# Optimization experiments

Measured on AMD Instinct MI355X. Metric: run time of the kernel, lower is better.

Reference implementation:

```python
import jax, jax.numpy as jnp
import numpy as np

B = 1_000_000   # reflections
K = 16_384      # groups
E = 64          # encoder_out
H = 64          # hidden_dim


def setup_inputs() -> dict:
    key = jax.random.key(0)
    ks = jax.random.split(key, 12)
    x = jax.random.normal(ks[0], (B, E), dtype=jnp.float32)
    gl = jax.random.randint(ks[1], (B,), 0, K)
    # guarantee every group id 0..K-1 appears, so torch.unique == arange(K)
    gl = gl.at[:K].set(jnp.arange(K))
    s = 0.05
    W1 = jax.random.normal(ks[2], (E, H), jnp.float32) * s
    b1 = jax.random.normal(ks[3], (H,), jnp.float32) * s
    W2 = jax.random.normal(ks[4], (H, H), jnp.float32) * s
    b2 = jax.random.normal(ks[5], (H,), jnp.float32) * s
    W3 = jax.random.normal(ks[6], (H, H), jnp.float32) * s
    b3 = jax.random.normal(ks[7], (H,), jnp.float32) * s
    w_mu = jax.random.normal(ks[8], (H, 1), jnp.float32) * s
    b_mu = jnp.full((1,), -6.9, jnp.float32)   # log_tau_init
    w_lv = jax.random.normal(ks[9], (H, 1), jnp.float32) * s
    b_lv = jnp.full((1,), -2.0, jnp.float32)
    return {"x": x, "group_labels": gl, "W1": W1, "b1": b1, "W2": W2, "b2": b2,
            "W3": W3, "b3": b3, "w_mu": w_mu, "b_mu": b_mu, "w_lv": w_lv, "b_lv": b_lv}


def reference(x, group_labels, W1, b1, W2, b2, W3, b3, w_mu, b_mu, w_lv, b_lv):
    # phi: Linear -> SiLU -> Linear -> SiLU
    z = jax.nn.silu(jax.nn.silu(x @ W1 + b1) @ W2 + b2)          # (B, H)
    # segment mean by group (math-equivalent to the dense one-hot matmul)
    counts = jax.ops.segment_sum(jnp.ones((z.shape[0],), z.dtype),
                                 group_labels, num_segments=K)    # (K,)
    gsum = jax.ops.segment_sum(z, group_labels, num_segments=K)   # (K, H)
    group_features = gsum / counts[:, None]
    # rho + heads
    h = jax.nn.silu(group_features @ W3 + b3)                     # (K, H)
    mu = (h @ w_mu + b_mu)[:, 0]                                  # (K,)
    logvar = jnp.clip((h @ w_lv + b_lv)[:, 0], -10.0, 4.0)        # (K,)
    std = jnp.exp(0.5 * logvar)
    eps = jax.random.normal(jax.random.key(42), std.shape, std.dtype)
    log_tau = mu + std * eps                                      # reparam sample
    tau_group = jnp.exp(log_tau)
    # unique_groups == arange(K) by construction -> searchsorted is identity
    tau_per_refl = tau_group[group_labels][:, None]               # (B, 1)
    log_tau_per_refl = log_tau[group_labels][:, None]             # (B, 1)
    return (mu, logvar, tau_per_refl, log_tau_per_refl)
```

## Files before the change

kernel.cpp:

```cpp
#include <hip/hip_runtime.h>

#define BN 1000000
#define KN 16384
#define HN 64
#define TPB 256
#define NW  4
#define NB  512
#define NCHUNK ((BN + TPB - 1) / TPB)

typedef __bf16 bf16x8 __attribute__((ext_vector_type(8)));
typedef float  f32x4  __attribute__((ext_vector_type(4)));
typedef unsigned short u16x8 __attribute__((ext_vector_type(8)));

__device__ __forceinline__ unsigned short f2bf(float f) {
    unsigned u = __float_as_uint(f);
    u += 0x7fffu + ((u >> 16) & 1u);
    return (unsigned short)(u >> 16);
}
__device__ __forceinline__ float bf2f(unsigned short b) {
    return __uint_as_float(((unsigned)b) << 16);
}
__device__ __forceinline__ float silu_f(float v) {
    return v * __builtin_amdgcn_rcpf(1.0f + __expf(-v));
}
__device__ __forceinline__ f32x4 mfma16(bf16x8 a, bf16x8 b, f32x4 c) {
    return __builtin_amdgcn_mfma_f32_16x16x32_bf16(a, b, c, 0, 0, 0);
}

__device__ __forceinline__ float erfinv_xla(float x) {
    float w = -log1pf(-x * x);
    float p;
    if (w < 5.0f) {
        w -= 2.5f;
        p = 2.81022636e-08f;
        p = fmaf(p, w, 3.43273939e-07f);
        p = fmaf(p, w, -3.5233877e-06f);
        p = fmaf(p, w, -4.39150654e-06f);
        p = fmaf(p, w, 0.00021858087f);
        p = fmaf(p, w, -0.00125372503f);
        p = fmaf(p, w, -0.00417768164f);
        p = fmaf(p, w, 0.246640727f);
        p = fmaf(p, w, 1.50140941f);
    } else {
        w = sqrtf(w) - 3.0f;
        p = -0.000200214257f;
        p = fmaf(p, w, 0.000100950558f);
        p = fmaf(p, w, 0.00134934322f);
        p = fmaf(p, w, -0.00367342844f);
        p = fmaf(p, w, 0.00573950773f);
        p = fmaf(p, w, -0.0076224613f);
        p = fmaf(p, w, 0.00943887047f);
        p = fmaf(p, w, 1.00167406f);
        p = fmaf(p, w, 2.83297682f);
    }
    return p * x;
}

__device__ __forceinline__ float jax_eps16384(int gid) {
    const unsigned k0 = 0u, k1 = 42u, k2 = 0x1BD11BDAu ^ 0u ^ 42u;
    unsigned x0 = 0u + k0;
    unsigned x1 = (unsigned)gid + k1;
#define TF_RND(r) { x0 += x1; x1 = (x1 << (r)) | (x1 >> (32 - (r))); x1 ^= x0; }
    TF_RND(13) TF_RND(15) TF_RND(26) TF_RND(6)  x0 += k1; x1 += k2 + 1u;
    TF_RND(17) TF_RND(29) TF_RND(16) TF_RND(24) x0 += k2; x1 += k0 + 2u;
    TF_RND(13) TF_RND(15) TF_RND(26) TF_RND(6)  x0 += k0; x1 += k1 + 3u;
    TF_RND(17) TF_RND(29) TF_RND(16) TF_RND(24) x0 += k1; x1 += k2 + 4u;
    TF_RND(13) TF_RND(15) TF_RND(26) TF_RND(6)  x0 += k2; x1 += k0 + 5u;
#undef TF_RND
    unsigned bits = x0 ^ x1;
    float f = __uint_as_float((bits >> 9) | 0x3f800000u) - 1.0f;
    const float mn = -0.99999994f;
    float u = fmaxf(f * 2.0f + mn, mn);
    return 1.41421354f * erfinv_xla(u);
}

__global__ __launch_bounds__(256) void k_count(const int* __restrict__ gl,
                                               int* __restrict__ counts,
                                               float4* __restrict__ gz) {
    int i = blockIdx.x * 256 + threadIdx.x;
    const float4 z4 = make_float4(0.f, 0.f, 0.f, 0.f);
    for (int j = i; j < KN * HN / 4; j += 250112) gz[j] = z4;
    if (i < BN / 4) {
        int4 g = ((const int4*)gl)[i];
        atomicAdd(&counts[g.x], 1); atomicAdd(&counts[g.y], 1);
        atomicAdd(&counts[g.z], 1); atomicAdd(&counts[g.w], 1);
    }
}

__global__ __launch_bounds__(1024) void k_scan(const int* __restrict__ counts, int* __restrict__ cursor) {
    __shared__ int wtot[16];
    const int t = threadIdx.x, lane = t & 63, wv = t >> 6;
    const int4* c4 = (const int4*)counts;
    int4 q0 = c4[t * 4], q1 = c4[t * 4 + 1], q2 = c4[t * 4 + 2], q3 = c4[t * 4 + 3];
    int c[16] = {q0.x, q0.y, q0.z, q0.w, q1.x, q1.y, q1.z, q1.w,
                 q2.x, q2.y, q2.z, q2.w, q3.x, q3.y, q3.z, q3.w};
    int loc[16], s = 0;
    #pragma unroll
    for (int i = 0; i < 16; ++i) { loc[i] = s; s += c[i]; }
    const int own = s;
    #pragma unroll
    for (int off = 1; off < 64; off <<= 1) {
        int v = __shfl_up(s, off);
        if (lane >= off) s += v;
    }
    if (lane == 63) wtot[wv] = s;
    __syncthreads();
    int wbase = 0;
    #pragma unroll
    for (int w = 0; w < 16; ++w) wbase += (w < wv) ? wtot[w] : 0;
    const int ebase = wbase + s - own;
    int o[16];
    #pragma unroll
    for (int i = 0; i < 16; ++i) o[i] = ebase + loc[i];
    int4* o4 = (int4*)cursor;
    o4[t * 4]     = make_int4(o[0],  o[1],  o[2],  o[3]);
    o4[t * 4 + 1] = make_int4(o[4],  o[5],  o[6],  o[7]);
    o4[t * 4 + 2] = make_int4(o[8],  o[9],  o[10], o[11]);
    o4[t * 4 + 3] = make_int4(o[12], o[13], o[14], o[15]);
}

__global__ __launch_bounds__(256) void k_scatter(const int* __restrict__ gl, int* __restrict__ cursor,
                                                 int2* __restrict__ spk) {
    int i = blockIdx.x * 256 + threadIdx.x;
    if (i < BN / 4) {
        int4 g = ((const int4*)gl)[i];
        int r = i * 4;
        int p0 = atomicAdd(&cursor[g.x], 1); spk[p0] = make_int2(r,     g.x);
        int p1 = atomicAdd(&cursor[g.y], 1); spk[p1] = make_int2(r + 1, g.y);
        int p2 = atomicAdd(&cursor[g.z], 1); spk[p2] = make_int2(r + 2, g.z);
        int p3 = atomicAdd(&cursor[g.w], 1); spk[p3] = make_int2(r + 3, g.w);
    }
}

__global__ __launch_bounds__(TPB, 2) void k_phase1(
    const float* __restrict__ x, const int2* __restrict__ spk,
    const float* __restrict__ W1, const float* __restrict__ b1,
    const float* __restrict__ W2, const float* __restrict__ b2,
    float* __restrict__ gsum)
{
    __shared__ __align__(16) unsigned short w1t[64 * 64];
    __shared__ __align__(16) unsigned short w2t[64 * 64];
    __shared__ __align__(16) unsigned short xh[NW][64 * 64];
    __shared__ float b1s[64], b2s[64];
    __shared__ int sg_s[NW][64];

    const int t = threadIdx.x;
    const int wv = t >> 6, lane = t & 63;
    const int lj = lane & 15, lg = lane >> 4;

    {
        const float4* W1v = (const float4*)W1;
        const float4* W2v = (const float4*)W2;
        #pragma unroll
        for (int i = 0; i < 4; ++i) {
            int e4 = i * 256 + t;
            int k  = e4 >> 4;
            int j0 = (e4 & 15) * 4;
            float4 a = W1v[e4];
            float4 b = W2v[e4];
            float av[4] = {a.x, a.y, a.z, a.w};
            float bv[4] = {b.x, b.y, b.z, b.w};
            #pragma unroll
            for (int c = 0; c < 4; ++c) {
                int j = j0 + c;
                int off = j * 128 + ((2 * k) ^ ((j & 7) << 4));
                *(unsigned short*)((char*)w1t + off) = f2bf(av[c]);
                *(unsigned short*)((char*)w2t + off) = f2bf(bv[c]);
            }
        }
        if (t < 64) { b1s[t] = b1[t]; b2s[t] = b2[t]; }
    }
    __syncthreads();

    float bc1[4], bc2[4];
    #pragma unroll
    for (int ct = 0; ct < 4; ++ct) { bc1[ct] = b1s[ct * 16 + lj]; bc2[ct] = b2s[ct * 16 + lj]; }

    unsigned short* myx = &xh[wv][0];
    int2   rsA[4], rsB[4];
    float4 xr[4][4];
    bf16x8 af[4][2];

    auto load_spk = [&](int c, int2 (&dst)[4]) {
        int cc = c < NCHUNK - 1 ? c : NCHUNK - 1;
        #pragma unroll
        for (int rt = 0; rt < 4; ++rt) {
            int r = cc * TPB + wv * 64 + rt * 16 + lj;
            dst[rt] = spk[r < BN ? r : BN - 1];
        }
    };
    auto load_x = [&](const int2 (&src)[4]) {
        #pragma unroll
        for (int rt = 0; rt < 4; ++rt) {
            const float* xp = x + (size_t)src[rt].x * 64 + lg * 8;
            xr[rt][0] = *(const float4*)(xp);
            xr[rt][1] = *(const float4*)(xp + 4);
            xr[rt][2] = *(const float4*)(xp + 32);
            xr[rt][3] = *(const float4*)(xp + 36);
        }
    };
    auto compute = [&]() {
        f32x4 acc[4][4];
        #pragma unroll
        for (int a = 0; a < 4; ++a)
            #pragma unroll
            for (int b = 0; b < 4; ++b) acc[a][b] = f32x4{0.f, 0.f, 0.f, 0.f};
        #pragma unroll
        for (int kk = 0; kk < 2; ++kk) {
            const int kbyte = kk * 64 + lg * 16;
            bf16x8 bw[4];
            #pragma unroll
            for (int ct = 0; ct < 4; ++ct) {
                int row = ct * 16 + lj;
                bw[ct] = *(const bf16x8*)((char*)w1t + row * 128 + (kbyte ^ ((row & 7) << 4)));
            }
            #pragma unroll
            for (int rt = 0; rt < 4; ++rt)
                #pragma unroll
                for (int ct = 0; ct < 4; ++ct)
                    acc[rt][ct] = mfma16(af[rt][kk], bw[ct], acc[rt][ct]);
        }
        #pragma unroll
        for (int rt = 0; rt < 4; ++rt) {
            #pragma unroll
            for (int ct = 0; ct < 4; ++ct) {
                f32x4 v = acc[rt][ct];
                #pragma unroll
                for (int rg = 0; rg < 4; ++rg) {
                    int row = rt * 16 + lg * 4 + rg;
                    int col = ct * 16 + lj;
                    float h = silu_f(v[rg] + bc1[ct]);
                    int off = row * 128 + ((2 * col) ^ ((row & 7) << 4));
                    *(unsigned short*)((char*)myx + off) = f2bf(h);
                }
                acc[rt][ct] = f32x4{0.f, 0.f, 0.f, 0.f};
            }
        }
        #pragma unroll
        for (int kk = 0; kk < 2; ++kk) {
            const int kbyte = kk * 64 + lg * 16;
            bf16x8 bw[4];
            #pragma unroll
            for (int ct = 0; ct < 4; ++ct) {
                int row = ct * 16 + lj;
                bw[ct] = *(const bf16x8*)((char*)w2t + row * 128 + (kbyte ^ ((row & 7) << 4)));
            }
            #pragma unroll
            for (int rt = 0; rt < 4; ++rt) {
                int row = rt * 16 + lj;
                bf16x8 aw = *(const bf16x8*)((char*)myx + row * 128 + (kbyte ^ ((row & 7) << 4)));
                #pragma unroll
                for (int ct = 0; ct < 4; ++ct)
                    acc[rt][ct] = mfma16(aw, bw[ct], acc[rt][ct]);
            }
        }
        #pragma unroll
        for (int rt = 0; rt < 4; ++rt) {
            #pragma unroll
            for (int ct = 0; ct < 4; ++ct) {
                f32x4 v = acc[rt][ct];
                int col  = ct * 16 + lj;
                int row0 = rt * 16 + lg * 4;
                ushort4 pk;
                pk.x = f2bf(silu_f(v[0] + bc2[ct]));
                pk.y = f2bf(silu_f(v[1] + bc2[ct]));
                pk.z = f2bf(silu_f(v[2] + bc2[ct]));
                pk.w = f2bf(silu_f(v[3] + bc2[ct]));
                *(ushort4*)((char*)myx + col * 128 + ((2 * row0) ^ ((col & 7) << 4))) = pk;
            }
        }
        {
            const int c = lane;
            const char* zT = (const char*)myx;
            float vsum = 0.0f;
            int curg = -2;
            #pragma unroll
            for (int blk = 0; blk < 8; ++blk) {
                u16x8 v = *(const u16x8*)(zT + c * 128 + ((16 * blk) ^ ((c & 7) << 4)));
                int4 ga = *(const int4*)(&sg_s[wv][blk * 8]);
                int4 gb = *(const int4*)(&sg_s[wv][blk * 8 + 4]);
                int gs[8] = {ga.x, ga.y, ga.z, ga.w, gb.x, gb.y, gb.z, gb.w};
                #pragma unroll
                for (int j = 0; j < 8; ++j) {
                    int g = gs[j];
                    if (g != curg) {
                        if (curg >= 0) atomicAdd(&gsum[curg * 64 + c], vsum);
                        vsum = 0.0f;
                        curg = g;
                    }
                    vsum += bf2f(v[j]);
                }
            }
            if (curg >= 0) atomicAdd(&gsum[curg * 64 + c], vsum);
        }
    };

    auto pstep = [&](int2 (&CUR)[4], int2 (&NXT)[4], int c) {
        if (lg == 0) {
            #pragma unroll
            for (int rt = 0; rt < 4; ++rt) {
                int r = c * TPB + wv * 64 + rt * 16 + lj;
                sg_s[wv][rt * 16 + lj] = (r < BN) ? CUR[rt].y : -1;
            }
        }
        #pragma unroll
        for (int rt = 0; rt < 4; ++rt)
            #pragma unroll
            for (int kk = 0; kk < 2; ++kk) {
                float4 a = xr[rt][kk * 2], b = xr[rt][kk * 2 + 1];
                u16x8 u;
                u[0] = f2bf(a.x); u[1] = f2bf(a.y); u[2] = f2bf(a.z); u[3] = f2bf(a.w);
                u[4] = f2bf(b.x); u[5] = f2bf(b.y); u[6] = f2bf(b.z); u[7] = f2bf(b.w);
                af[rt][kk] = __builtin_bit_cast(bf16x8, u);
            }
        load_x(NXT);
        load_spk(c + 2 * NB, CUR);
        compute();
    };

    const int c0 = blockIdx.x;
    load_spk(c0, rsA);
    load_spk(c0 + NB, rsB);
    load_x(rsA);

    int c = c0;
    while (true) {
        pstep(rsA, rsB, c); c += NB; if (c >= NCHUNK) break;
        pstep(rsB, rsA, c); c += NB; if (c >= NCHUNK) break;
    }
}

__global__ __launch_bounds__(64) void k_phase2(
    const float* __restrict__ gsum, const int* __restrict__ counts,
    const float* __restrict__ W3, const float* __restrict__ b3,
    const float* __restrict__ wmu, const float* __restrict__ bmu,
    const float* __restrict__ wlv, const float* __restrict__ blv,
    float* __restrict__ out, float* __restrict__ taug, float* __restrict__ ltaug)
{
    __shared__ __align__(16) float w3t[64 * 64];
    __shared__ float b3s[64], wmus[64], wlvs[64];
    const int t = threadIdx.x;
    for (int i = 0; i < 64; ++i) w3t[t * 64 + i] = W3[i * 64 + t];
    b3s[t] = b3[t]; wmus[t] = wmu[t]; wlvs[t] = wlv[t];
    __syncthreads();

    const int gid = blockIdx.x * 64 + t;
    const float inv = 1.0f / (float)counts[gid];
    float gf[64];
    #pragma unroll
    for (int i = 0; i < 16; ++i) {
        float4 v = *(const float4*)(gsum + (size_t)gid * 64 + i * 4);
        gf[i * 4 + 0] = v.x * inv; gf[i * 4 + 1] = v.y * inv;
        gf[i * 4 + 2] = v.z * inv; gf[i * 4 + 3] = v.w * inv;
    }
    float mu = bmu[0], lv = blv[0];
    for (int j = 0; j < 64; ++j) {
        float a = b3s[j];
        const float4* wr = (const float4*)(w3t + j * 64);
        #pragma unroll
        for (int k = 0; k < 16; ++k) {
            float4 wv = wr[k];
            a += gf[k * 4 + 0] * wv.x + gf[k * 4 + 1] * wv.y
               + gf[k * 4 + 2] * wv.z + gf[k * 4 + 3] * wv.w;
        }
        float h = silu_f(a);
        mu += h * wmus[j];
        lv += h * wlvs[j];
    }
    lv = fminf(fmaxf(lv, -10.0f), 4.0f);
    float sd  = __expf(0.5f * lv);
    float eps = jax_eps16384(gid);
    float lt  = mu + sd * eps;
    out[gid]      = mu;
    out[KN + gid] = lv;
    taug[gid]  = __expf(lt);
    ltaug[gid] = lt;
}

__global__ __launch_bounds__(256) void k_phase3(
    const int* __restrict__ gl, const float* __restrict__ taug,
    const float* __restrict__ ltaug, float* __restrict__ out)
{
    int i = blockIdx.x * 256 + threadIdx.x;
    if (i < BN / 4) {
        int4 g = ((const int4*)gl)[i];
        float4 tv = make_float4(taug[g.x],  taug[g.y],  taug[g.z],  taug[g.w]);
        float4 lv = make_float4(ltaug[g.x], ltaug[g.y], ltaug[g.z], ltaug[g.w]);
        ((float4*)(out + 2 * KN))[i]      = tv;
        ((float4*)(out + 2 * KN + BN))[i] = lv;
    }
}

extern "C" void kernel_launch(void* const* d_in, const int* in_sizes, int n_in,
                              void* d_out, int out_size, void* d_ws, size_t ws_size,
                              hipStream_t stream)
{
    const float* x   = (const float*)d_in[0];
    const int*   gl  = (const int*)d_in[1];
    const float* W1  = (const float*)d_in[2];
    const float* b1  = (const float*)d_in[3];
    const float* W2  = (const float*)d_in[4];
    const float* b2  = (const float*)d_in[5];
    const float* W3  = (const float*)d_in[6];
    const float* b3  = (const float*)d_in[7];
    const float* wmu = (const float*)d_in[8];
    const float* bmu = (const float*)d_in[9];
    const float* wlv = (const float*)d_in[10];
    const float* blv = (const float*)d_in[11];
    float* out = (float*)d_out;

    float* ws     = (float*)d_ws;
    float* gsum   = ws;
    int*   counts = (int*)(gsum + KN * HN);
    int*   cursor = counts + KN;
    float* taug   = (float*)(cursor + KN);
    float* ltaug  = taug + KN;
    int2*  spk    = (int2*)(ltaug + KN);

    hipMemsetAsync(counts, 0, (size_t)KN * sizeof(int), stream);

    const int nb4 = (BN / 4 + 255) / 256;
    k_count  <<<nb4, 256, 0, stream>>>(gl, counts, (float4*)gsum);
    k_scan   <<<1, 1024, 0, stream>>>(counts, cursor);
    k_scatter<<<nb4, 256, 0, stream>>>(gl, cursor, spk);
    k_phase1 <<<NB, TPB, 0, stream>>>(x, spk, W1, b1, W2, b2, gsum);
    k_phase2 <<<KN / 64, 64, 0, stream>>>(gsum, counts, W3, b3, wmu, bmu, wlv, blv, out, taug, ltaug);
    k_phase3 <<<nb4, 256, 0, stream>>>(gl, taug, ltaug, out);
}
```

Measured before the change: 250.1 us.

## Drop x register prefetch and raise phase1 occupancy to three blocks per CU

Removes the software pipeline that held the next chunk's x rows in registers across the compute step. Now x is loaded at the start of each iteration, and only the sorted index pairs are prefetched one step ahead. Register pressure falls, which allows launch bounds of 3 blocks per SM/CU, and the grid grows from 512 to 768 blocks to match. The aim is to hide gather latency through more resident waves rather than in-thread prefetch. The risk is exposed load latency inside each wave if occupancy does not rise enough.

```diff
diff --git a/kernel.cpp b/kernel.cpp
--- a/kernel.cpp
+++ b/kernel.cpp
@@ -5,7 +5,7 @@
 #define HN 64
 #define TPB 256
 #define NW  4
-#define NB  512
+#define NB  768
 #define NCHUNK ((BN + TPB - 1) / TPB)
 
 typedef __bf16 bf16x8 __attribute__((ext_vector_type(8)));
@@ -132,7 +132,7 @@
     }
 }
 
-__global__ __launch_bounds__(TPB, 2) void k_phase1(
+__global__ __launch_bounds__(TPB, 3) void k_phase1(
     const float* __restrict__ x, const int2* __restrict__ spk,
     const float* __restrict__ W1, const float* __restrict__ b1,
     const float* __restrict__ W2, const float* __restrict__ b2,
@@ -177,9 +177,7 @@
     for (int ct = 0; ct < 4; ++ct) { bc1[ct] = b1s[ct * 16 + lj]; bc2[ct] = b2s[ct * 16 + lj]; }
 
     unsigned short* myx = &xh[wv][0];
-    int2   rsA[4], rsB[4];
-    float4 xr[4][4];
-    bf16x8 af[4][2];
+    int2 rsA[4], rsB[4];
 
     auto load_spk = [&](int c, int2 (&dst)[4]) {
         int cc = c < NCHUNK - 1 ? c : NCHUNK - 1;
@@ -189,17 +187,37 @@
             dst[rt] = spk[r < BN ? r : BN - 1];
         }
     };
-    auto load_x = [&](const int2 (&src)[4]) {
+
+    auto iter = [&](int2 (&CUR)[4], int2 (&NXT)[4], int c) {
+        float4 xr[4][4];
         #pragma unroll
         for (int rt = 0; rt < 4; ++rt) {
-            const float* xp = x + (size_t)src[rt].x * 64 + lg * 8;
+            const float* xp = x + (size_t)CUR[rt].x * 64 + lg * 8;
             xr[rt][0] = *(const float4*)(xp);
             xr[rt][1] = *(const float4*)(xp + 4);
             xr[rt][2] = *(const float4*)(xp + 32);
             xr[rt][3] = *(const float4*)(xp + 36);
         }
-    };
-    auto compute = [&]() {
+        load_spk(c + NB, NXT);
+        if (lg == 0) {
+            #pragma unroll
+            for (int rt = 0; rt < 4; ++rt) {
+                int r = c * TPB + wv * 64 + rt * 16 + lj;
+                sg_s[wv][rt * 16 + lj] = (r < BN) ? CUR[rt].y : -1;
+            }
+        }
+        bf16x8 af[4][2];
+        #pragma unroll
+        for (int rt = 0; rt < 4; ++rt)
+            #pragma unroll
+            for (int kk = 0; kk < 2; ++kk) {
+                float4 a = xr[rt][kk * 2], b = xr[rt][kk * 2 + 1];
+                u16x8 u;
+                u[0] = f2bf(a.x); u[1] = f2bf(a.y); u[2] = f2bf(a.z); u[3] = f2bf(a.w);
+                u[4] = f2bf(b.x); u[5] = f2bf(b.y); u[6] = f2bf(b.z); u[7] = f2bf(b.w);
+                af[rt][kk] = __builtin_bit_cast(bf16x8, u);
+            }
+
         f32x4 acc[4][4];
         #pragma unroll
         for (int a = 0; a < 4; ++a)
@@ -270,13 +288,13 @@
             }
         }
         {
-            const int c = lane;
+            const int c2 = lane;
             const char* zT = (const char*)myx;
             float vsum = 0.0f;
             int curg = -2;
             #pragma unroll
             for (int blk = 0; blk < 8; ++blk) {
-                u16x8 v = *(const u16x8*)(zT + c * 128 + ((16 * blk) ^ ((c & 7) << 4)));
+                u16x8 v = *(const u16x8*)(zT + c2 * 128 + ((16 * blk) ^ ((c2 & 7) << 4)));
                 int4 ga = *(const int4*)(&sg_s[wv][blk * 8]);
                 int4 gb = *(const int4*)(&sg_s[wv][blk * 8 + 4]);
                 int gs[8] = {ga.x, ga.y, ga.z, ga.w, gb.x, gb.y, gb.z, gb.w};
@@ -284,49 +302,22 @@
                 for (int j = 0; j < 8; ++j) {
                     int g = gs[j];
                     if (g != curg) {
-                        if (curg >= 0) atomicAdd(&gsum[curg * 64 + c], vsum);
+                        if (curg >= 0) atomicAdd(&gsum[curg * 64 + c2], vsum);
                         vsum = 0.0f;
                         curg = g;
                     }
                     vsum += bf2f(v[j]);
                 }
             }
-            if (curg >= 0) atomicAdd(&gsum[curg * 64 + c], vsum);
+            if (curg >= 0) atomicAdd(&gsum[curg * 64 + c2], vsum);
         }
     };
 
-    auto pstep = [&](int2 (&CUR)[4], int2 (&NXT)[4], int c) {
-        if (lg == 0) {
-            #pragma unroll
-            for (int rt = 0; rt < 4; ++rt) {
-                int r = c * TPB + wv * 64 + rt * 16 + lj;
-                sg_s[wv][rt * 16 + lj] = (r < BN) ? CUR[rt].y : -1;
-            }
-        }
-        #pragma unroll
-        for (int rt = 0; rt < 4; ++rt)
-            #pragma unroll
-            for (int kk = 0; kk < 2; ++kk) {
-                float4 a = xr[rt][kk * 2], b = xr[rt][kk * 2 + 1];
-                u16x8 u;
-                u[0] = f2bf(a.x); u[1] = f2bf(a.y); u[2] = f2bf(a.z); u[3] = f2bf(a.w);
-                u[4] = f2bf(b.x); u[5] = f2bf(b.y); u[6] = f2bf(b.z); u[7] = f2bf(b.w);
-                af[rt][kk] = __builtin_bit_cast(bf16x8, u);
-            }
-        load_x(NXT);
-        load_spk(c + 2 * NB, CUR);
-        compute();
-    };
-
-    const int c0 = blockIdx.x;
-    load_spk(c0, rsA);
-    load_spk(c0 + NB, rsB);
-    load_x(rsA);
-
-    int c = c0;
+    int c = blockIdx.x;
+    load_spk(c, rsA);
     while (true) {
-        pstep(rsA, rsB, c); c += NB; if (c >= NCHUNK) break;
-        pstep(rsB, rsA, c); c += NB; if (c >= NCHUNK) break;
+        iter(rsA, rsB, c); c += NB; if (c >= NCHUNK) break;
+        iter(rsB, rsA, c); c += NB; if (c >= NCHUNK) break;
     }
 }
 
```

New measurement: 319.8 us. 27.9% more time.

## Fuse all phases into one persistent kernel with software grid barriers

Applied to the files above, without the earlier changes.

Replaces six separate launches (count, scan, scatter, MLP phase, group head, gather) with one persistent 512-block kernel that separates stages with an atomic generation-counter grid barrier. The aim is to remove launch gaps and per-kernel tail effects. In exchange the count, scatter and gather loops now run on only 512 blocks, the scan runs in a single 256-thread block, and the group head uses 64 blocks of 256 threads. Correctness also relies on all 512 blocks being co-resident. The bf16 conversions are also switched to compiler builtins.

```diff
diff --git a/kernel.cpp b/kernel.cpp
--- a/kernel.cpp
+++ b/kernel.cpp
@@ -5,7 +5,7 @@
 #define HN 64
 #define TPB 256
 #define NW  4
-#define NB  512
+#define NBLK 512
 #define NCHUNK ((BN + TPB - 1) / TPB)
 
 typedef __bf16 bf16x8 __attribute__((ext_vector_type(8)));
@@ -13,12 +13,10 @@
 typedef unsigned short u16x8 __attribute__((ext_vector_type(8)));
 
 __device__ __forceinline__ unsigned short f2bf(float f) {
-    unsigned u = __float_as_uint(f);
-    u += 0x7fffu + ((u >> 16) & 1u);
-    return (unsigned short)(u >> 16);
+    return __builtin_bit_cast(unsigned short, (__bf16)f);
 }
 __device__ __forceinline__ float bf2f(unsigned short b) {
-    return __uint_as_float(((unsigned)b) << 16);
+    return (float)__builtin_bit_cast(__bf16, b);
 }
 __device__ __forceinline__ float silu_f(float v) {
     return v * __builtin_amdgcn_rcpf(1.0f + __expf(-v));
@@ -74,69 +72,37 @@
     return 1.41421354f * erfinv_xla(u);
 }
 
-__global__ __launch_bounds__(256) void k_count(const int* __restrict__ gl,
-                                               int* __restrict__ counts,
-                                               float4* __restrict__ gz) {
-    int i = blockIdx.x * 256 + threadIdx.x;
-    const float4 z4 = make_float4(0.f, 0.f, 0.f, 0.f);
-    for (int j = i; j < KN * HN / 4; j += 250112) gz[j] = z4;
-    if (i < BN / 4) {
-        int4 g = ((const int4*)gl)[i];
-        atomicAdd(&counts[g.x], 1); atomicAdd(&counts[g.y], 1);
-        atomicAdd(&counts[g.z], 1); atomicAdd(&counts[g.w], 1);
-    }
-}
-
-__global__ __launch_bounds__(1024) void k_scan(const int* __restrict__ counts, int* __restrict__ cursor) {
-    __shared__ int wtot[16];
-    const int t = threadIdx.x, lane = t & 63, wv = t >> 6;
-    const int4* c4 = (const int4*)counts;
-    int4 q0 = c4[t * 4], q1 = c4[t * 4 + 1], q2 = c4[t * 4 + 2], q3 = c4[t * 4 + 3];
-    int c[16] = {q0.x, q0.y, q0.z, q0.w, q1.x, q1.y, q1.z, q1.w,
-                 q2.x, q2.y, q2.z, q2.w, q3.x, q3.y, q3.z, q3.w};
-    int loc[16], s = 0;
-    #pragma unroll
-    for (int i = 0; i < 16; ++i) { loc[i] = s; s += c[i]; }
-    const int own = s;
-    #pragma unroll
-    for (int off = 1; off < 64; off <<= 1) {
-        int v = __shfl_up(s, off);
-        if (lane >= off) s += v;
-    }
-    if (lane == 63) wtot[wv] = s;
+__device__ __forceinline__ void gridbar(int* bar) {
     __syncthreads();
-    int wbase = 0;
-    #pragma unroll
-    for (int w = 0; w < 16; ++w) wbase += (w < wv) ? wtot[w] : 0;
-    const int ebase = wbase + s - own;
-    int o[16];
-    #pragma unroll
-    for (int i = 0; i < 16; ++i) o[i] = ebase + loc[i];
-    int4* o4 = (int4*)cursor;
-    o4[t * 4]     = make_int4(o[0],  o[1],  o[2],  o[3]);
-    o4[t * 4 + 1] = make_int4(o[4],  o[5],  o[6],  o[7]);
-    o4[t * 4 + 2] = make_int4(o[8],  o[9],  o[10], o[11]);
-    o4[t * 4 + 3] = make_int4(o[12], o[13], o[14], o[15]);
-}
-
-__global__ __launch_bounds__(256) void k_scatter(const int* __restrict__ gl, int* __restrict__ cursor,
-                                                 int2* __restrict__ spk) {
-    int i = blockIdx.x * 256 + threadIdx.x;
-    if (i < BN / 4) {
-        int4 g = ((const int4*)gl)[i];
-        int r = i * 4;
-        int p0 = atomicAdd(&cursor[g.x], 1); spk[p0] = make_int2(r,     g.x);
-        int p1 = atomicAdd(&cursor[g.y], 1); spk[p1] = make_int2(r + 1, g.y);
-        int p2 = atomicAdd(&cursor[g.z], 1); spk[p2] = make_int2(r + 2, g.z);
-        int p3 = atomicAdd(&cursor[g.w], 1); spk[p3] = make_int2(r + 3, g.w);
-    }
-}
-
-__global__ __launch_bounds__(TPB, 2) void k_phase1(
-    const float* __restrict__ x, const int2* __restrict__ spk,
+    if (threadIdx.x == 0) {
+        __threadfence();
+        int* cnt = bar;
+        int* gen = bar + 1;
+        int g = __hip_atomic_load(gen, __ATOMIC_ACQUIRE, __HIP_MEMORY_SCOPE_AGENT);
+        int a = __hip_atomic_fetch_add(cnt, 1, __ATOMIC_ACQ_REL, __HIP_MEMORY_SCOPE_AGENT);
+        if (a == NBLK - 1) {
+            __hip_atomic_store(cnt, 0, __ATOMIC_RELAXED, __HIP_MEMORY_SCOPE_AGENT);
+            __hip_atomic_fetch_add(gen, 1, __ATOMIC_RELEASE, __HIP_MEMORY_SCOPE_AGENT);
+        } else {
+            while (__hip_atomic_load(gen, __ATOMIC_ACQUIRE, __HIP_MEMORY_SCOPE_AGENT) == g)
+                __builtin_amdgcn_s_sleep(1);
+        }
+        __threadfence();
+    }
+    __syncthreads();
+}
+
+__global__ __launch_bounds__(TPB, 2) void k_mega(
+    const float* __restrict__ x, const int* __restrict__ gl,
     const float* __restrict__ W1, const float* __restrict__ b1,
     const float* __restrict__ W2, const float* __restrict__ b2,
-    float* __restrict__ gsum)
+    const float* __restrict__ W3, const float* __restrict__ b3,
+    const float* __restrict__ wmu, const float* __restrict__ bmu,
+    const float* __restrict__ wlv, const float* __restrict__ blv,
+    float* __restrict__ out,
+    float* __restrict__ gsum, int* __restrict__ counts, int* __restrict__ cursor,
+    float* __restrict__ taug, float* __restrict__ ltaug,
+    int2* __restrict__ spk, int* __restrict__ bar)
 {
     __shared__ __align__(16) unsigned short w1t[64 * 64];
     __shared__ __align__(16) unsigned short w2t[64 * 64];
@@ -147,6 +113,7 @@
     const int t = threadIdx.x;
     const int wv = t >> 6, lane = t & 63;
     const int lj = lane & 15, lg = lane >> 4;
+    const int gtid = blockIdx.x * TPB + t;
 
     {
         const float4* W1v = (const float4*)W1;
@@ -170,219 +137,270 @@
         }
         if (t < 64) { b1s[t] = b1[t]; b2s[t] = b2[t]; }
     }
-    __syncthreads();
-
-    float bc1[4], bc2[4];
-    #pragma unroll
-    for (int ct = 0; ct < 4; ++ct) { bc1[ct] = b1s[ct * 16 + lj]; bc2[ct] = b2s[ct * 16 + lj]; }
-
-    unsigned short* myx = &xh[wv][0];
-    int2   rsA[4], rsB[4];
-    float4 xr[4][4];
-    bf16x8 af[4][2];
-
-    auto load_spk = [&](int c, int2 (&dst)[4]) {
-        int cc = c < NCHUNK - 1 ? c : NCHUNK - 1;
-        #pragma unroll
-        for (int rt = 0; rt < 4; ++rt) {
-            int r = cc * TPB + wv * 64 + rt * 16 + lj;
-            dst[rt] = spk[r < BN ? r : BN - 1];
-        }
-    };
-    auto load_x = [&](const int2 (&src)[4]) {
-        #pragma unroll
-        for (int rt = 0; rt < 4; ++rt) {
-            const float* xp = x + (size_t)src[rt].x * 64 + lg * 8;
-            xr[rt][0] = *(const float4*)(xp);
-            xr[rt][1] = *(const float4*)(xp + 4);
-            xr[rt][2] = *(const float4*)(xp + 32);
-            xr[rt][3] = *(const float4*)(xp + 36);
-        }
-    };
-    auto compute = [&]() {
-        f32x4 acc[4][4];
-        #pragma unroll
-        for (int a = 0; a < 4; ++a)
-            #pragma unroll
-            for (int b = 0; b < 4; ++b) acc[a][b] = f32x4{0.f, 0.f, 0.f, 0.f};
-        #pragma unroll
-        for (int kk = 0; kk < 2; ++kk) {
-            const int kbyte = kk * 64 + lg * 16;
-            bf16x8 bw[4];
-            #pragma unroll
-            for (int ct = 0; ct < 4; ++ct) {
-                int row = ct * 16 + lj;
-                bw[ct] = *(const bf16x8*)((char*)w1t + row * 128 + (kbyte ^ ((row & 7) << 4)));
+
+    {
+        if (gtid < KN / 4) ((int4*)counts)[gtid] = make_int4(0, 0, 0, 0);
+        const float4 z4 = make_float4(0.f, 0.f, 0.f, 0.f);
+        #pragma unroll
+        for (int i = 0; i < 2; ++i) {
+            int j = i * (NBLK * TPB) + gtid;
+            if (j < KN * HN / 4) ((float4*)gsum)[j] = z4;
+        }
+    }
+    gridbar(bar);
+
+    for (int i = gtid; i < BN / 4; i += NBLK * TPB) {
+        int4 g = ((const int4*)gl)[i];
+        atomicAdd(&counts[g.x], 1); atomicAdd(&counts[g.y], 1);
+        atomicAdd(&counts[g.z], 1); atomicAdd(&counts[g.w], 1);
+    }
+    gridbar(bar);
+
+    if (blockIdx.x == 0) {
+        const int4* cc4 = (const int4*)counts;
+        int tsum = 0;
+        #pragma unroll
+        for (int i = 0; i < 16; ++i) {
+            int4 q = cc4[t * 16 + i];
+            tsum += q.x + q.y + q.z + q.w;
+        }
+        int inc = tsum;
+        #pragma unroll
+        for (int off = 1; off < 64; off <<= 1) {
+            int v = __shfl_up(inc, off);
+            if (lane >= off) inc += v;
+        }
+        if (lane == 63) sg_s[0][wv] = inc;
+        __syncthreads();
+        int wb = 0;
+        #pragma unroll
+        for (int w = 0; w < 4; ++w) wb += (w < wv) ? sg_s[0][w] : 0;
+        int run = wb + inc - tsum;
+        int4* cu4 = (int4*)cursor;
+        #pragma unroll
+        for (int i = 0; i < 16; ++i) {
+            int4 q = cc4[t * 16 + i];
+            int4 o;
+            o.x = run; o.y = run + q.x; o.z = o.y + q.y; o.w = o.z + q.z;
+            run = o.w + q.w;
+            cu4[t * 16 + i] = o;
+        }
+    }
+    gridbar(bar);
+
+    for (int i = gtid; i < BN / 4; i += NBLK * TPB) {
+        int4 g = ((const int4*)gl)[i];
+        int r = i * 4;
+        int p0 = atomicAdd(&cursor[g.x], 1); spk[p0] = make_int2(r,     g.x);
+        int p1 = atomicAdd(&cursor[g.y], 1); spk[p1] = make_int2(r + 1, g.y);
+        int p2 = atomicAdd(&cursor[g.z], 1); spk[p2] = make_int2(r + 2, g.z);
+        int p3 = atomicAdd(&cursor[g.w], 1); spk[p3] = make_int2(r + 3, g.w);
+    }
+    gridbar(bar);
+
+    {
+        float bc1[4], bc2[4];
+        #pragma unroll
+        for (int ct = 0; ct < 4; ++ct) { bc1[ct] = b1s[ct * 16 + lj]; bc2[ct] = b2s[ct * 16 + lj]; }
+
+        unsigned short* myx = &xh[wv][0];
+        int2   rsA[4], rsB[4];
+        float4 xr[4][4];
+        bf16x8 af[4][2];
+
+        auto load_spk = [&](int c, int2 (&dst)[4]) {
+            int cc = c < NCHUNK - 1 ? c : NCHUNK - 1;
+            #pragma unroll
+            for (int rt = 0; rt < 4; ++rt) {
+                int r = cc * TPB + wv * 64 + rt * 16 + lj;
+                dst[rt] = spk[r < BN ? r : BN - 1];
+            }
+        };
+        auto load_x = [&](const int2 (&src)[4]) {
+            #pragma unroll
+            for (int rt = 0; rt < 4; ++rt) {
+                const float* xp = x + (size_t)src[rt].x * 64 + lg * 8;
+                xr[rt][0] = *(const float4*)(xp);
+                xr[rt][1] = *(const float4*)(xp + 4);
+                xr[rt][2] = *(const float4*)(xp + 32);
+                xr[rt][3] = *(const float4*)(xp + 36);
+            }
+        };
+        auto compute = [&]() {
+            f32x4 acc[4][4];
+            #pragma unroll
+            for (int a = 0; a < 4; ++a)
+                #pragma unroll
+                for (int b = 0; b < 4; ++b) acc[a][b] = f32x4{0.f, 0.f, 0.f, 0.f};
+            #pragma unroll
+            for (int kk = 0; kk < 2; ++kk) {
+                const int kbyte = kk * 64 + lg * 16;
+                bf16x8 bw[4];
+                #pragma unroll
+                for (int ct = 0; ct < 4; ++ct) {
+                    int row = ct * 16 + lj;
+                    bw[ct] = *(const bf16x8*)((char*)w1t + row * 128 + (kbyte ^ ((row & 7) << 4)));
+                }
+                #pragma unroll
+                for (int rt = 0; rt < 4; ++rt)
+                    #pragma unroll
+                    for (int ct = 0; ct < 4; ++ct)
+                        acc[rt][ct] = mfma16(af[rt][kk], bw[ct], acc[rt][ct]);
+            }
+            #pragma unroll
+            for (int rt = 0; rt < 4; ++rt) {
+                #pragma unroll
+                for (int ct = 0; ct < 4; ++ct) {
+                    f32x4 v = acc[rt][ct];
+                    #pragma unroll
+                    for (int rg = 0; rg < 4; ++rg) {
+                        int row = rt * 16 + lg * 4 + rg;
+                        int col = ct * 16 + lj;
+                        float h = silu_f(v[rg] + bc1[ct]);
+                        int off = row * 128 + ((2 * col) ^ ((row & 7) << 4));
+                        *(unsigned short*)((char*)myx + off) = f2bf(h);
+                    }
+                    acc[rt][ct] = f32x4{0.f, 0.f, 0.f, 0.f};
+                }
+            }
+            #pragma unroll
+            for (int kk = 0; kk < 2; ++kk) {
+                const int kbyte = kk * 64 + lg * 16;
+                bf16x8 bw[4];
+                #pragma unroll
+                for (int ct = 0; ct < 4; ++ct) {
+                    int row = ct * 16 + lj;
+                    bw[ct] = *(const bf16x8*)((char*)w2t + row * 128 + (kbyte ^ ((row & 7) << 4)));
+                }
+                #pragma unroll
+                for (int rt = 0; rt < 4; ++rt) {
+                    int row = rt * 16 + lj;
+                    bf16x8 aw = *(const bf16x8*)((char*)myx + row * 128 + (kbyte ^ ((row & 7) << 4)));
+                    #pragma unroll
+                    for (int ct = 0; ct < 4; ++ct)
+                        acc[rt][ct] = mfma16(aw, bw[ct], acc[rt][ct]);
+                }
+            }
+            #pragma unroll
+            for (int rt = 0; rt < 4; ++rt) {
+                #pragma unroll
+                for (int ct = 0; ct < 4; ++ct) {
+                    f32x4 v = acc[rt][ct];
+                    int col  = ct * 16 + lj;
+                    int row0 = rt * 16 + lg * 4;
+                    ushort4 pk;
+                    pk.x = f2bf(silu_f(v[0] + bc2[ct]));
+                    pk.y = f2bf(silu_f(v[1] + bc2[ct]));
+                    pk.z = f2bf(silu_f(v[2] + bc2[ct]));
+                    pk.w = f2bf(silu_f(v[3] + bc2[ct]));
+                    *(ushort4*)((char*)myx + col * 128 + ((2 * row0) ^ ((col & 7) << 4))) = pk;
+                }
+            }
+            {
+                const int c2 = lane;
+                const char* zT = (const char*)myx;
+                float vsum = 0.0f;
+                int curg = -2;
+                #pragma unroll
+                for (int blk = 0; blk < 8; ++blk) {
+                    u16x8 v = *(const u16x8*)(zT + c2 * 128 + ((16 * blk) ^ ((c2 & 7) << 4)));
+                    int4 ga = *(const int4*)(&sg_s[wv][blk * 8]);
+                    int4 gb = *(const int4*)(&sg_s[wv][blk * 8 + 4]);
+                    int gs[8] = {ga.x, ga.y, ga.z, ga.w, gb.x, gb.y, gb.z, gb.w};
+                    #pragma unroll
+                    for (int j = 0; j < 8; ++j) {
+                        int g = gs[j];
+                        if (g != curg) {
+                            if (curg >= 0) atomicAdd(&gsum[curg * 64 + c2], vsum);
+                            vsum = 0.0f;
+                            curg = g;
+                        }
+                        vsum += bf2f(v[j]);
+                    }
+                }
+                if (curg >= 0) atomicAdd(&gsum[curg * 64 + c2], vsum);
+            }
+        };
+        auto pstep = [&](int2 (&CUR)[4], int2 (&NXT)[4], int c) {
+            if (lg == 0) {
+                #pragma unroll
+                for (int rt = 0; rt < 4; ++rt) {
+                    int r = c * TPB + wv * 64 + rt * 16 + lj;
+                    sg_s[wv][rt * 16 + lj] = (r < BN) ? CUR[rt].y : -1;
+                }
             }
             #pragma unroll
             for (int rt = 0; rt < 4; ++rt)
                 #pragma unroll
-                for (int ct = 0; ct < 4; ++ct)
-                    acc[rt][ct] = mfma16(af[rt][kk], bw[ct], acc[rt][ct]);
-        }
-        #pragma unroll
-        for (int rt = 0; rt < 4; ++rt) {
-            #pragma unroll
-            for (int ct = 0; ct < 4; ++ct) {
-                f32x4 v = acc[rt][ct];
-                #pragma unroll
-                for (int rg = 0; rg < 4; ++rg) {
-                    int row = rt * 16 + lg * 4 + rg;
-                    int col = ct * 16 + lj;
-                    float h = silu_f(v[rg] + bc1[ct]);
-                    int off = row * 128 + ((2 * col) ^ ((row & 7) << 4));
-                    *(unsigned short*)((char*)myx + off) = f2bf(h);
-                }
-                acc[rt][ct] = f32x4{0.f, 0.f, 0.f, 0.f};
-            }
-        }
-        #pragma unroll
-        for (int kk = 0; kk < 2; ++kk) {
-            const int kbyte = kk * 64 + lg * 16;
-            bf16x8 bw[4];
-            #pragma unroll
-            for (int ct = 0; ct < 4; ++ct) {
-                int row = ct * 16 + lj;
-                bw[ct] = *(const bf16x8*)((char*)w2t + row * 128 + (kbyte ^ ((row & 7) << 4)));
-            }
-            #pragma unroll
-            for (int rt = 0; rt < 4; ++rt) {
-                int row = rt * 16 + lj;
-                bf16x8 aw = *(const bf16x8*)((char*)myx + row * 128 + (kbyte ^ ((row & 7) << 4)));
-                #pragma unroll
-                for (int ct = 0; ct < 4; ++ct)
-                    acc[rt][ct] = mfma16(aw, bw[ct], acc[rt][ct]);
-            }
-        }
-        #pragma unroll
-        for (int rt = 0; rt < 4; ++rt) {
-            #pragma unroll
-            for (int ct = 0; ct < 4; ++ct) {
-                f32x4 v = acc[rt][ct];
-                int col  = ct * 16 + lj;
-                int row0 = rt * 16 + lg * 4;
-                ushort4 pk;
-                pk.x = f2bf(silu_f(v[0] + bc2[ct]));
-                pk.y = f2bf(silu_f(v[1] + bc2[ct]));
-                pk.z = f2bf(silu_f(v[2] + bc2[ct]));
-                pk.w = f2bf(silu_f(v[3] + bc2[ct]));
-                *(ushort4*)((char*)myx + col * 128 + ((2 * row0) ^ ((col & 7) << 4))) = pk;
-            }
-        }
-        {
-            const int c = lane;
-            const char* zT = (const char*)myx;
-            float vsum = 0.0f;
-            int curg = -2;
-            #pragma unroll
-            for (int blk = 0; blk < 8; ++blk) {
-                u16x8 v = *(const u16x8*)(zT + c * 128 + ((16 * blk) ^ ((c & 7) << 4)));
-                int4 ga = *(const int4*)(&sg_s[wv][blk * 8]);
-                int4 gb = *(const int4*)(&sg_s[wv][blk * 8 + 4]);
-                int gs[8] = {ga.x, ga.y, ga.z, ga.w, gb.x, gb.y, gb.z, gb.w};
-                #pragma unroll
-                for (int j = 0; j < 8; ++j) {
-                    int g = gs[j];
-                    if (g != curg) {
-                        if (curg >= 0) atomicAdd(&gsum[curg * 64 + c], vsum);
-                        vsum = 0.0f;
-                        curg = g;
-                    }
-                    vsum += bf2f(v[j]);
-                }
-            }
-            if (curg >= 0) atomicAdd(&gsum[curg * 64 + c], vsum);
-        }
-    };
-
-    auto pstep = [&](int2 (&CUR)[4], int2 (&NXT)[4], int c) {
-        if (lg == 0) {
-            #pragma unroll
-            for (int rt = 0; rt < 4; ++rt) {
-                int r = c * TPB + wv * 64 + rt * 16 + lj;
-                sg_s[wv][rt * 16 + lj] = (r < BN) ? CUR[rt].y : -1;
-            }
-        }
-        #pragma unroll
-        for (int rt = 0; rt < 4; ++rt)
-            #pragma unroll
-            for (int kk = 0; kk < 2; ++kk) {
-                float4 a = xr[rt][kk * 2], b = xr[rt][kk * 2 + 1];
-                u16x8 u;
-                u[0] = f2bf(a.x); u[1] = f2bf(a.y); u[2] = f2bf(a.z); u[3] = f2bf(a.w);
-                u[4] = f2bf(b.x); u[5] = f2bf(b.y); u[6] = f2bf(b.z); u[7] = f2bf(b.w);
-                af[rt][kk] = __builtin_bit_cast(bf16x8, u);
-            }
-        load_x(NXT);
-        load_spk(c + 2 * NB, CUR);
-        compute();
-    };
-
-    const int c0 = blockIdx.x;
-    load_spk(c0, rsA);
-    load_spk(c0 + NB, rsB);
-    load_x(rsA);
-
-    int c = c0;
-    while (true) {
-        pstep(rsA, rsB, c); c += NB; if (c >= NCHUNK) break;
-        pstep(rsB, rsA, c); c += NB; if (c >= NCHUNK) break;
-    }
-}
-
-__global__ __launch_bounds__(64) void k_phase2(
-    const float* __restrict__ gsum, const int* __restrict__ counts,
-    const float* __restrict__ W3, const float* __restrict__ b3,
-    const float* __restrict__ wmu, const float* __restrict__ bmu,
-    const float* __restrict__ wlv, const float* __restrict__ blv,
-    float* __restrict__ out, float* __restrict__ taug, float* __restrict__ ltaug)
-{
-    __shared__ __align__(16) float w3t[64 * 64];
-    __shared__ float b3s[64], wmus[64], wlvs[64];
-    const int t = threadIdx.x;
-    for (int i = 0; i < 64; ++i) w3t[t * 64 + i] = W3[i * 64 + t];
-    b3s[t] = b3[t]; wmus[t] = wmu[t]; wlvs[t] = wlv[t];
-    __syncthreads();
-
-    const int gid = blockIdx.x * 64 + t;
-    const float inv = 1.0f / (float)counts[gid];
-    float gf[64];
-    #pragma unroll
-    for (int i = 0; i < 16; ++i) {
-        float4 v = *(const float4*)(gsum + (size_t)gid * 64 + i * 4);
-        gf[i * 4 + 0] = v.x * inv; gf[i * 4 + 1] = v.y * inv;
-        gf[i * 4 + 2] = v.z * inv; gf[i * 4 + 3] = v.w * inv;
-    }
-    float mu = bmu[0], lv = blv[0];
-    for (int j = 0; j < 64; ++j) {
-        float a = b3s[j];
-        const float4* wr = (const float4*)(w3t + j * 64);
-        #pragma unroll
-        for (int k = 0; k < 16; ++k) {
-            float4 wv = wr[k];
-            a += gf[k * 4 + 0] * wv.x + gf[k * 4 + 1] * wv.y
-               + gf[k * 4 + 2] * wv.z + gf[k * 4 + 3] * wv.w;
-        }
-        float h = silu_f(a);
-        mu += h * wmus[j];
-        lv += h * wlvs[j];
-    }
-    lv = fminf(fmaxf(lv, -10.0f), 4.0f);
-    float sd  = __expf(0.5f * lv);
-    float eps = jax_eps16384(gid);
-    float lt  = mu + sd * eps;
-    out[gid]      = mu;
-    out[KN + gid] = lv;
-    taug[gid]  = __expf(lt);
-    ltaug[gid] = lt;
-}
-
-__global__ __launch_bounds__(256) void k_phase3(
-    const int* __restrict__ gl, const float* __restrict__ taug,
-    const float* __restrict__ ltaug, float* __restrict__ out)
-{
-    int i = blockIdx.x * 256 + threadIdx.x;
-    if (i < BN / 4) {
+                for (int kk = 0; kk < 2; ++kk) {
+                    float4 a = xr[rt][kk * 2], b = xr[rt][kk * 2 + 1];
+                    u16x8 u;
+                    u[0] = f2bf(a.x); u[1] = f2bf(a.y); u[2] = f2bf(a.z); u[3] = f2bf(a.w);
+                    u[4] = f2bf(b.x); u[5] = f2bf(b.y); u[6] = f2bf(b.z); u[7] = f2bf(b.w);
+                    af[rt][kk] = __builtin_bit_cast(bf16x8, u);
+                }
+            load_x(NXT);
+            load_spk(c + 2 * NBLK, CUR);
+            compute();
+        };
+
+        const int c0 = blockIdx.x;
+        load_spk(c0, rsA);
+        load_spk(c0 + NBLK, rsB);
+        load_x(rsA);
+        int c = c0;
+        while (true) {
+            pstep(rsA, rsB, c); c += NBLK; if (c >= NCHUNK) break;
+            pstep(rsB, rsA, c); c += NBLK; if (c >= NCHUNK) break;
+        }
+    }
+    gridbar(bar);
+
+    if (blockIdx.x < KN / TPB) {
+        float* w3f = (float*)&xh[0][0];
+        const int j = t & 63, q = t >> 6;
+        #pragma unroll
+        for (int i = 0; i < 16; ++i) {
+            int k = q * 16 + i;
+            w3f[j * 64 + k] = W3[k * 64 + j];
+        }
+        __syncthreads();
+
+        const int gid = blockIdx.x * TPB + t;
+        const float inv = 1.0f / (float)counts[gid];
+        float gf[64];
+        #pragma unroll
+        for (int i = 0; i < 16; ++i) {
+            float4 v = *(const float4*)(gsum + (size_t)gid * 64 + i * 4);
+            gf[i * 4 + 0] = v.x * inv; gf[i * 4 + 1] = v.y * inv;
+            gf[i * 4 + 2] = v.z * inv; gf[i * 4 + 3] = v.w * inv;
+        }
+        float mu = bmu[0], lv = blv[0];
+        for (int jj = 0; jj < 64; ++jj) {
+            float a = b3[jj];
+            const float4* wr = (const float4*)(w3f + jj * 64);
+            #pragma unroll
+            for (int k = 0; k < 16; ++k) {
+                float4 wvv = wr[k];
+                a += gf[k * 4 + 0] * wvv.x + gf[k * 4 + 1] * wvv.y
+                   + gf[k * 4 + 2] * wvv.z + gf[k * 4 + 3] * wvv.w;
+            }
+            float h = silu_f(a);
+            mu += h * wmu[jj];
+            lv += h * wlv[jj];
+        }
+        lv = fminf(fmaxf(lv, -10.0f), 4.0f);
+        float sd  = __expf(0.5f * lv);
+        float eps = jax_eps16384(gid);
+        float lt  = mu + sd * eps;
+        out[gid]      = mu;
+        out[KN + gid] = lv;
+        taug[gid]  = __expf(lt);
+        ltaug[gid] = lt;
+    }
+    gridbar(bar);
+
+    for (int i = gtid; i < BN / 4; i += NBLK * TPB) {
         int4 g = ((const int4*)gl)[i];
         float4 tv = make_float4(taug[g.x],  taug[g.y],  taug[g.z],  taug[g.w]);
         float4 lv = make_float4(ltaug[g.x], ltaug[g.y], ltaug[g.z], ltaug[g.w]);
@@ -416,14 +434,9 @@
     float* taug   = (float*)(cursor + KN);
     float* ltaug  = taug + KN;
     int2*  spk    = (int2*)(ltaug + KN);
-
-    hipMemsetAsync(counts, 0, (size_t)KN * sizeof(int), stream);
-
-    const int nb4 = (BN / 4 + 255) / 256;
-    k_count  <<<nb4, 256, 0, stream>>>(gl, counts, (float4*)gsum);
-    k_scan   <<<1, 1024, 0, stream>>>(counts, cursor);
-    k_scatter<<<nb4, 256, 0, stream>>>(gl, cursor, spk);
-    k_phase1 <<<NB, TPB, 0, stream>>>(x, spk, W1, b1, W2, b2, gsum);
-    k_phase2 <<<KN / 64, 64, 0, stream>>>(gsum, counts, W3, b3, wmu, bmu, wlv, blv, out, taug, ltaug);
-    k_phase3 <<<nb4, 256, 0, stream>>>(gl, taug, ltaug, out);
-}
+    int*   bar    = (int*)(spk + BN);
+
+    hipMemsetAsync(bar, 0, 2 * sizeof(int), stream);
+    k_mega<<<NBLK, TPB, 0, stream>>>(x, gl, W1, b1, W2, b2, W3, b3, wmu, bmu, wlv, blv,
+                                     out, gsum, counts, cursor, taug, ltaug, spk, bar);
+}
```

Result: slower. 720.3 us (+188.0%).
